# Optimization experiments

Hardware: AMD Instinct MI355X
Metric: run time of the kernel (lower is better)

Reference implementation:

```python
import jax, jax.numpy as jnp
import numpy as np

S, C1, C2, N = 4096, 2048, 2048, 1024


def setup_inputs() -> dict:
    key = jax.random.key(0)
    k1, k2, k3, k4 = jax.random.split(key, 4)
    # child log-likelihoods (samples, child_nodes); modest scale so exp() stays finite,
    # matching the (numerically naive) torch forward which exps without max-subtraction.
    ll1 = jax.random.normal(k1, (S, C1), dtype=jnp.float32)
    ll2 = jax.random.normal(k2, (S, C2), dtype=jnp.float32)
    # log edge weights, one tensor per child layer: (nodes, child_nodes)
    w1 = jax.random.normal(k3, (N, C1), dtype=jnp.float32)
    w2 = jax.random.normal(k4, (N, C2), dtype=jnp.float32)
    return {"ll1": ll1, "ll2": ll2, "w1": w1, "w2": w2}


def reference(ll1, ll2, w1, w2):
    # Per child layer: sum_c exp(ll[s,c] + w[n,c]) == exp(ll) @ exp(w).T  -> (S, N)
    # (same math as unsqueeze/repeat/exp/sum in the torch code, without the (S,C,N) blowup)
    result = jnp.exp(ll1) @ jnp.exp(w1).T + jnp.exp(ll2) @ jnp.exp(w2).T  # (S, N)
    # per-node log normalization constant over concatenated weights
    log_z = jax.nn.logsumexp(jnp.concatenate([w1, w2], axis=1), axis=1)  # (N,)
    return jnp.log(result) - log_z[None, :]
```

## Files before the change

kernel.cpp:

```cpp
#include <hip/hip_runtime.h>

#define S_DIM 4096
#define C_DIM 2048
#define N_DIM 1024
#define K_DIM 4096

#define BM 128
#define BN 128
#define BK 32
#define NT (K_DIM / BK)
#define BUF_BYTES 16384
#define NBUF 3

typedef __attribute__((ext_vector_type(8))) short bf16x8;
typedef __attribute__((ext_vector_type(4))) float f32x4;

__device__ static inline unsigned short f2bf(float f) {
    unsigned int u = __float_as_uint(f);
    u += 0x7FFFu + ((u >> 16) & 1u);
    return (unsigned short)(u >> 16);
}

__global__ void exp_ll_kernel(const float* __restrict__ ll1,
                              const float* __restrict__ ll2,
                              unsigned short* __restrict__ A) {
    const int total4 = S_DIM * C_DIM / 4;
    int stride = gridDim.x * blockDim.x;
    for (int i = blockIdx.x * blockDim.x + threadIdx.x; i < total4; i += stride) {
        int e = i << 2;
        int r = e >> 11;
        int c = e & 2047;
        size_t dst = ((size_t)r << 12) + c;
        float4 v = *reinterpret_cast<const float4*>(ll1 + e);
        ushort4 o;
        o.x = f2bf(__expf(v.x)); o.y = f2bf(__expf(v.y));
        o.z = f2bf(__expf(v.z)); o.w = f2bf(__expf(v.w));
        *reinterpret_cast<ushort4*>(A + dst) = o;
        float4 u = *reinterpret_cast<const float4*>(ll2 + e);
        ushort4 p;
        p.x = f2bf(__expf(u.x)); p.y = f2bf(__expf(u.y));
        p.z = f2bf(__expf(u.z)); p.w = f2bf(__expf(u.w));
        *reinterpret_cast<ushort4*>(A + dst + C_DIM) = p;
    }
}

__global__ void w_kernel(const float* __restrict__ w1,
                         const float* __restrict__ w2,
                         unsigned short* __restrict__ B,
                         float* __restrict__ lz) {
    const int n = blockIdx.x;
    const int tid = threadIdx.x;
    const int lane = tid & 63, wv = tid >> 6;
    const float* r1 = w1 + ((size_t)n << 11);
    const float* r2 = w2 + ((size_t)n << 11);
    float4 v0 = *reinterpret_cast<const float4*>(r1 + tid * 8);
    float4 v1 = *reinterpret_cast<const float4*>(r1 + tid * 8 + 4);
    float4 u0 = *reinterpret_cast<const float4*>(r2 + tid * 8);
    float4 u1 = *reinterpret_cast<const float4*>(r2 + tid * 8 + 4);

    float mx = fmaxf(fmaxf(fmaxf(v0.x, v0.y), fmaxf(v0.z, v0.w)),
                     fmaxf(fmaxf(v1.x, v1.y), fmaxf(v1.z, v1.w)));
    mx = fmaxf(mx, fmaxf(fmaxf(fmaxf(u0.x, u0.y), fmaxf(u0.z, u0.w)),
                          fmaxf(fmaxf(u1.x, u1.y), fmaxf(u1.z, u1.w))));
    #pragma unroll
    for (int off = 32; off > 0; off >>= 1) mx = fmaxf(mx, __shfl_xor(mx, off));
    __shared__ float red[4];
    if (lane == 0) red[wv] = mx;
    __syncthreads();
    mx = fmaxf(fmaxf(red[0], red[1]), fmaxf(red[2], red[3]));

    float s = __expf(v0.x - mx) + __expf(v0.y - mx) + __expf(v0.z - mx) + __expf(v0.w - mx)
            + __expf(v1.x - mx) + __expf(v1.y - mx) + __expf(v1.z - mx) + __expf(v1.w - mx)
            + __expf(u0.x - mx) + __expf(u0.y - mx) + __expf(u0.z - mx) + __expf(u0.w - mx)
            + __expf(u1.x - mx) + __expf(u1.y - mx) + __expf(u1.z - mx) + __expf(u1.w - mx);
    #pragma unroll
    for (int off = 32; off > 0; off >>= 1) s += __shfl_xor(s, off);
    __syncthreads();
    __shared__ float red2[4];
    if (lane == 0) red2[wv] = s;
    __syncthreads();
    if (tid == 0)
        lz[n] = mx + __logf(red2[0] + red2[1] + red2[2] + red2[3]);

    unsigned short* brow = B + ((size_t)n << 12);
    ushort4 o;
    o.x = f2bf(__expf(v0.x)); o.y = f2bf(__expf(v0.y));
    o.z = f2bf(__expf(v0.z)); o.w = f2bf(__expf(v0.w));
    *reinterpret_cast<ushort4*>(brow + tid * 8) = o;
    o.x = f2bf(__expf(v1.x)); o.y = f2bf(__expf(v1.y));
    o.z = f2bf(__expf(v1.z)); o.w = f2bf(__expf(v1.w));
    *reinterpret_cast<ushort4*>(brow + tid * 8 + 4) = o;
    o.x = f2bf(__expf(u0.x)); o.y = f2bf(__expf(u0.y));
    o.z = f2bf(__expf(u0.z)); o.w = f2bf(__expf(u0.w));
    *reinterpret_cast<ushort4*>(brow + C_DIM + tid * 8) = o;
    o.x = f2bf(__expf(u1.x)); o.y = f2bf(__expf(u1.y));
    o.z = f2bf(__expf(u1.z)); o.w = f2bf(__expf(u1.w));
    *reinterpret_cast<ushort4*>(brow + C_DIM + tid * 8 + 4) = o;
}

typedef const unsigned int __attribute__((address_space(1)))* gas_ptr;
typedef unsigned int __attribute__((address_space(3)))* las_ptr;

__global__ __launch_bounds__(256) void gemm_log_kernel(
        const unsigned short* __restrict__ A,
        const unsigned short* __restrict__ B,
        const float* __restrict__ lz,
        float* __restrict__ out) {
    __shared__ __align__(16) char lds[NBUF * BUF_BYTES];
    const int tid  = threadIdx.x;
    const int l    = tid & 63;
    const int w    = tid >> 6;
    const int bn = blockIdx.x & 7;
    const int bm = blockIdx.x >> 3;
    const int wr = w >> 1, wc = w & 1;
    const int lcol = l & 15, lk = l >> 4;

    const int kg = (l & 3) ^ ((l >> 3) & 3);
    const unsigned short* sA[2]; const unsigned short* sB[2];
    int dA[2], dB[2];
    #pragma unroll
    for (int i = 0; i < 2; ++i) {
        const int s   = i * 4 + w;
        const int row = s * 16 + (l >> 2);
        sA[i] = A + (size_t)(bm * BM + row) * K_DIM + kg * 8;
        sB[i] = B + (size_t)(bn * BN + row) * K_DIM + kg * 8;
        dA[i] = s * 1024;
        dB[i] = 8192 + s * 1024;
    }

    const int swz = (lk ^ ((lcol >> 1) & 3)) << 4;
    int aoff[4], boff[4];
    #pragma unroll
    for (int m = 0; m < 4; ++m) {
        aoff[m] = (wr * 64 + m * 16 + lcol) * 64 + swz;
        boff[m] = 8192 + (wc * 64 + m * 16 + lcol) * 64 + swz;
    }

    f32x4 acc[4][4] = {};

#define GLOAD(src, off) __builtin_amdgcn_global_load_lds((gas_ptr)(const void*)(src), \
        (las_ptr)(void*)(lds + (off)), 16, 0, 0)
#define STAGE(kt, bufb) { const int _ko = (kt) * BK; const int _bo = (bufb) * BUF_BYTES; \
        GLOAD(sA[0] + _ko, _bo + dA[0]); GLOAD(sA[1] + _ko, _bo + dA[1]);               \
        GLOAD(sB[0] + _ko, _bo + dB[0]); GLOAD(sB[1] + _ko, _bo + dB[1]); }

    STAGE(0, 0);
    STAGE(1, 1);
    int bufi = 0, buf2 = 2;
    for (int t = 0; t < NT; ++t) {
        if (t == NT - 1) { asm volatile("s_waitcnt vmcnt(0)" ::: "memory"); }
        else             { asm volatile("s_waitcnt vmcnt(4)" ::: "memory"); }
        __builtin_amdgcn_s_barrier();
        if (t + 2 < NT) STAGE(t + 2, buf2);

        const char* base = lds + bufi * BUF_BYTES;
        bf16x8 a[4], b[4];
        #pragma unroll
        for (int m = 0; m < 4; ++m) a[m] = *reinterpret_cast<const bf16x8*>(base + aoff[m]);
        #pragma unroll
        for (int n = 0; n < 4; ++n) b[n] = *reinterpret_cast<const bf16x8*>(base + boff[n]);
        #pragma unroll
        for (int m = 0; m < 4; ++m)
            #pragma unroll
            for (int n = 0; n < 4; ++n)
                acc[m][n] = __builtin_amdgcn_mfma_f32_16x16x32_bf16(a[m], b[n], acc[m][n], 0, 0, 0);

        bufi = (bufi == 2) ? 0 : bufi + 1;
        buf2 = (buf2 == 2) ? 0 : buf2 + 1;
    }
#undef STAGE
#undef GLOAD

    const int col_base = bn * BN + wc * 64;
    float lzv[4];
    #pragma unroll
    for (int n = 0; n < 4; ++n) lzv[n] = lz[col_base + n * 16 + lcol];
    #pragma unroll
    for (int m = 0; m < 4; ++m) {
        const int row0 = bm * BM + wr * 64 + m * 16 + lk * 4;
        #pragma unroll
        for (int n = 0; n < 4; ++n) {
            const int col = col_base + n * 16 + lcol;
            #pragma unroll
            for (int j = 0; j < 4; ++j)
                out[(size_t)(row0 + j) * N_DIM + col] = __logf(acc[m][n][j]) - lzv[n];
        }
    }
}

__global__ void naive_kernel(const float* __restrict__ ll1, const float* __restrict__ ll2,
                             const float* __restrict__ w1, const float* __restrict__ w2,
                             float* __restrict__ out) {
    int idx = blockIdx.x * blockDim.x + threadIdx.x;
    if (idx >= S_DIM * N_DIM) return;
    int s = idx >> 10, n = idx & (N_DIM - 1);
    const float* a1 = ll1 + (size_t)s * C_DIM;
    const float* a2 = ll2 + (size_t)s * C_DIM;
    const float* b1 = w1 + (size_t)n * C_DIM;
    const float* b2 = w2 + (size_t)n * C_DIM;
    float mx = -3.0e38f;
    for (int c = 0; c < C_DIM; ++c) mx = fmaxf(mx, b1[c]);
    for (int c = 0; c < C_DIM; ++c) mx = fmaxf(mx, b2[c]);
    float zs = 0.f, acc = 0.f;
    for (int c = 0; c < C_DIM; ++c) { zs += __expf(b1[c] - mx); acc += __expf(a1[c] + b1[c]); }
    for (int c = 0; c < C_DIM; ++c) { zs += __expf(b2[c] - mx); acc += __expf(a2[c] + b2[c]); }
    out[idx] = __logf(acc) - (mx + __logf(zs));
}

extern "C" void kernel_launch(void* const* d_in, const int* in_sizes, int n_in,
                              void* d_out, int out_size, void* d_ws, size_t ws_size,
                              hipStream_t stream) {
    const float* ll1 = (const float*)d_in[0];
    const float* ll2 = (const float*)d_in[1];
    const float* w1  = (const float*)d_in[2];
    const float* w2  = (const float*)d_in[3];
    float* out = (float*)d_out;

    const size_t a_elems = (size_t)S_DIM * K_DIM;
    const size_t b_elems = (size_t)N_DIM * K_DIM;
    const size_t need = (a_elems + b_elems) * sizeof(unsigned short) + N_DIM * sizeof(float);
    if (ws_size < need) {
        naive_kernel<<<(S_DIM * N_DIM + 255) / 256, 256, 0, stream>>>(ll1, ll2, w1, w2, out);
        return;
    }
    unsigned short* Aws = (unsigned short*)d_ws;
    unsigned short* Bws = Aws + a_elems;
    float* lzws = (float*)(Bws + b_elems);

    exp_ll_kernel<<<2048, 256, 0, stream>>>(ll1, ll2, Aws);
    w_kernel<<<N_DIM, 256, 0, stream>>>(w1, w2, Bws, lzws);
    gemm_log_kernel<<<S_DIM / BM * (N_DIM / BN), 256, 0, stream>>>(Aws, Bws, lzws, out);
}
```

Baseline: 82.90 us.

## Halve GEMM M-tile to 64 and unroll triple-buffered K loop

```diff
diff --git a/kernel.cpp b/kernel.cpp
--- a/kernel.cpp
+++ b/kernel.cpp
@@ -5,11 +5,11 @@
 #define N_DIM 1024
 #define K_DIM 4096
 
-#define BM 128
+#define BM 64
 #define BN 128
 #define BK 32
 #define NT (K_DIM / BK)
-#define BUF_BYTES 16384
+#define TILE_BYTES 12288
 #define NBUF 3
 
 typedef __attribute__((ext_vector_type(8))) short bf16x8;
@@ -75,7 +75,6 @@
             + __expf(u1.x - mx) + __expf(u1.y - mx) + __expf(u1.z - mx) + __expf(u1.w - mx);
     #pragma unroll
     for (int off = 32; off > 0; off >>= 1) s += __shfl_xor(s, off);
-    __syncthreads();
     __shared__ float red2[4];
     if (lane == 0) red2[wv] = s;
     __syncthreads();
@@ -106,68 +105,66 @@
         const unsigned short* __restrict__ B,
         const float* __restrict__ lz,
         float* __restrict__ out) {
-    __shared__ __align__(16) char lds[NBUF * BUF_BYTES];
+    __shared__ __align__(16) char lds[NBUF * TILE_BYTES];
     const int tid  = threadIdx.x;
     const int l    = tid & 63;
     const int w    = tid >> 6;
     const int bn = blockIdx.x & 7;
     const int bm = blockIdx.x >> 3;
-    const int wr = w >> 1, wc = w & 1;
+    const int wr = w & 1, wc = w >> 1;
     const int lcol = l & 15, lk = l >> 4;
 
     const int kg = (l & 3) ^ ((l >> 3) & 3);
-    const unsigned short* sA[2]; const unsigned short* sB[2];
-    int dA[2], dB[2];
-    #pragma unroll
-    for (int i = 0; i < 2; ++i) {
-        const int s   = i * 4 + w;
-        const int row = s * 16 + (l >> 2);
-        sA[i] = A + (size_t)(bm * BM + row) * K_DIM + kg * 8;
-        sB[i] = B + (size_t)(bn * BN + row) * K_DIM + kg * 8;
-        dA[i] = s * 1024;
-        dB[i] = 8192 + s * 1024;
+    const unsigned short* src[3];
+    int dst[3];
+    #pragma unroll
+    for (int g = 0; g < 3; ++g) {
+        const int row = g * 64 + w * 16 + (l >> 2);
+        src[g] = (g == 0)
+            ? A + (size_t)(bm * BM + row) * K_DIM + kg * 8
+            : B + (size_t)(bn * BN + row - 64) * K_DIM + kg * 8;
+        dst[g] = row * 64 + (l & 3) * 16;
     }
 
     const int swz = (lk ^ ((lcol >> 1) & 3)) << 4;
-    int aoff[4], boff[4];
-    #pragma unroll
-    for (int m = 0; m < 4; ++m) {
-        aoff[m] = (wr * 64 + m * 16 + lcol) * 64 + swz;
-        boff[m] = 8192 + (wc * 64 + m * 16 + lcol) * 64 + swz;
-    }
-
-    f32x4 acc[4][4] = {};
-
-#define GLOAD(src, off) __builtin_amdgcn_global_load_lds((gas_ptr)(const void*)(src), \
-        (las_ptr)(void*)(lds + (off)), 16, 0, 0)
-#define STAGE(kt, bufb) { const int _ko = (kt) * BK; const int _bo = (bufb) * BUF_BYTES; \
-        GLOAD(sA[0] + _ko, _bo + dA[0]); GLOAD(sA[1] + _ko, _bo + dA[1]);               \
-        GLOAD(sB[0] + _ko, _bo + dB[0]); GLOAD(sB[1] + _ko, _bo + dB[1]); }
+    int aoff[2], boff[4];
+    #pragma unroll
+    for (int m = 0; m < 2; ++m) aoff[m] = (wr * 32 + m * 16 + lcol) * 64 + swz;
+    #pragma unroll
+    for (int n = 0; n < 4; ++n) boff[n] = 4096 + (wc * 64 + n * 16 + lcol) * 64 + swz;
+
+    f32x4 acc[2][4] = {};
+
+#define GLOAD(p, o) __builtin_amdgcn_global_load_lds((gas_ptr)(const void*)(p), \
+        (las_ptr)(void*)(lds + (o)), 16, 0, 0)
+#define STAGE(T, BUFB) { const int _ko = (T) * BK; const int _bo = (BUFB) * TILE_BYTES; \
+        GLOAD(src[0] + _ko, _bo + dst[0]); GLOAD(src[1] + _ko, _bo + dst[1]);           \
+        GLOAD(src[2] + _ko, _bo + dst[2]); }
+#define BODY(T, BUF, BUFS, WAITN, DOSTAGE) {                                            \
+        asm volatile("s_waitcnt vmcnt(" #WAITN ")" ::: "memory");                       \
+        __builtin_amdgcn_s_barrier();                                                   \
+        if (DOSTAGE) STAGE((T) + 2, BUFS);                                              \
+        const char* base = lds + (BUF) * TILE_BYTES;                                    \
+        bf16x8 a[2], b[4];                                                              \
+        _Pragma("unroll") for (int m = 0; m < 2; ++m)                                   \
+            a[m] = *reinterpret_cast<const bf16x8*>(base + aoff[m]);                    \
+        _Pragma("unroll") for (int n = 0; n < 4; ++n)                                   \
+            b[n] = *reinterpret_cast<const bf16x8*>(base + boff[n]);                    \
+        _Pragma("unroll") for (int m = 0; m < 2; ++m)                                   \
+            _Pragma("unroll") for (int n = 0; n < 4; ++n)                               \
+                acc[m][n] = __builtin_amdgcn_mfma_f32_16x16x32_bf16(a[m], b[n],         \
+                                                                   acc[m][n], 0, 0, 0); }
 
     STAGE(0, 0);
     STAGE(1, 1);
-    int bufi = 0, buf2 = 2;
-    for (int t = 0; t < NT; ++t) {
-        if (t == NT - 1) { asm volatile("s_waitcnt vmcnt(0)" ::: "memory"); }
-        else             { asm volatile("s_waitcnt vmcnt(4)" ::: "memory"); }
-        __builtin_amdgcn_s_barrier();
-        if (t + 2 < NT) STAGE(t + 2, buf2);
-
-        const char* base = lds + bufi * BUF_BYTES;
-        bf16x8 a[4], b[4];
-        #pragma unroll
-        for (int m = 0; m < 4; ++m) a[m] = *reinterpret_cast<const bf16x8*>(base + aoff[m]);
-        #pragma unroll
-        for (int n = 0; n < 4; ++n) b[n] = *reinterpret_cast<const bf16x8*>(base + boff[n]);
-        #pragma unroll
-        for (int m = 0; m < 4; ++m)
-            #pragma unroll
-            for (int n = 0; n < 4; ++n)
-                acc[m][n] = __builtin_amdgcn_mfma_f32_16x16x32_bf16(a[m], b[n], acc[m][n], 0, 0, 0);
-
-        bufi = (bufi == 2) ? 0 : bufi + 1;
-        buf2 = (buf2 == 2) ? 0 : buf2 + 1;
-    }
+    for (int t3 = 0; t3 < NT - 2; t3 += 3) {
+        BODY(t3 + 0, 0, 2, 3, 1);
+        BODY(t3 + 1, 1, 0, 3, 1);
+        BODY(t3 + 2, 2, 1, 3, 1);
+    }
+    BODY(NT - 2, 0, 2, 3, 0);
+    BODY(NT - 1, 1, 0, 0, 0);
+#undef BODY
 #undef STAGE
 #undef GLOAD
 
@@ -176,8 +173,8 @@
     #pragma unroll
     for (int n = 0; n < 4; ++n) lzv[n] = lz[col_base + n * 16 + lcol];
     #pragma unroll
-    for (int m = 0; m < 4; ++m) {
-        const int row0 = bm * BM + wr * 64 + m * 16 + lk * 4;
+    for (int m = 0; m < 2; ++m) {
+        const int row0 = bm * BM + wr * 32 + m * 16 + lk * 4;
         #pragma unroll
         for (int n = 0; n < 4; ++n) {
             const int col = col_base + n * 16 + lcol;
@@ -229,5 +226,5 @@
 
     exp_ll_kernel<<<2048, 256, 0, stream>>>(ll1, ll2, Aws);
     w_kernel<<<N_DIM, 256, 0, stream>>>(w1, w2, Bws, lzws);
-    gemm_log_kernel<<<S_DIM / BM * (N_DIM / BN), 256, 0, stream>>>(Aws, Bws, lzws, out);
-}
+    gemm_log_kernel<<<(S_DIM / BM) * (N_DIM / BN), 256, 0, stream>>>(Aws, Bws, lzws, out);
+}
```

After: 82.29 us. About the same (-0.7%).
